# Kernel tuning notes

Measured on AMD Instinct MI355X. Metric: run time of the kernel, lower is better.

## Reference

```python
import jax, jax.numpy as jnp
import numpy as np

N, L, H, K, T = 768, 8, 64, 4, 3

def _mlp2(x, w1, b1, w2, b2):
    # Linear -> ReLU -> Linear -> ReLU (matches nn.Sequential in q/k/v MLPs)
    return jax.nn.relu(jax.nn.relu(x @ w1 + b1) @ w2 + b2)

def setup_inputs() -> dict:
    key = jax.random.key(0)
    ks = jax.random.split(key, 20)
    s = 1.0 / np.sqrt(H)
    def lin(k, din, dout):
        return jax.random.uniform(k, (din, dout), jnp.float32, -s, s)
    def bias(k, dout):
        return jax.random.uniform(k, (dout,), jnp.float32, -s, s)
    inp = {
        "h": jax.random.normal(ks[0], (N, L, H), jnp.float32),
        "coord": jax.random.normal(ks[1], (N, L, K, T), jnp.float32),
        "wq1": lin(ks[2], H, H), "bq1": bias(ks[3], H),
        "wq2": lin(ks[4], H, H), "bq2": bias(ks[5], H),
        "wk1": lin(ks[6], H, H), "bk1": bias(ks[7], H),
        "wk2": lin(ks[8], H, H), "bk2": bias(ks[9], H),
        "wv1": lin(ks[10], H, H), "bv1": bias(ks[11], H),
        "wv2": lin(ks[12], H, H), "bv2": bias(ks[13], H),
        "wc1": lin(ks[14], H, H), "bc1": bias(ks[15], H),
        # final coord layer: Linear(H, 4, bias=False), xavier gain=0.001
        "wc2": jax.random.normal(ks[16], (H, K), jnp.float32) * 0.001,
    }
    return inp

def reference(h, coord, wq1, bq1, wq2, bq2, wk1, bk1, wk2, bk2,
              wv1, bv1, wv2, bv2, wc1, bc1, wc2):
    q = _mlp2(h, wq1, bq1, wq2, bq2)          # [N, L, H]
    k = _mlp2(h, wk1, bk1, wk2, bk2)          # [N, L, H]
    v = _mlp2(h, wv1, bv1, wv2, bv2)          # [N, L, H]
    # scores[i, j, l] = <q_i, k_j> per frame l; softmax over neighbor axis j (dim=1)
    scores = jnp.einsum('ilh,jlh->ijl', q, k)
    alpha = jax.nn.softmax(scores, axis=1)     # [N, N, L]
    h_agg = jnp.einsum('ijl,jlh->ilh', alpha, v)
    cmv = jax.nn.relu(v @ wc1 + bc1) @ wc2     # coord_mlp(v): [N, L, 4]
    coord_diff = coord[:, None] - coord[None]  # [N, N, L, 4, 3]
    x_agg = jnp.einsum('ijlkt,ijl,jlk->ilkt', coord_diff, alpha, cmv)
    return (h + h_agg, coord + x_agg)
```

## Files before the change

kernel.cpp:

```cpp
#include <hip/hip_runtime.h>
#include <hip/hip_bf16.h>

#define NN 768
#define LL 8
#define HH 64
#define IT 16
#define SCP 772
#define ABP 776

typedef __attribute__((ext_vector_type(8))) short bf16x8;
typedef __attribute__((ext_vector_type(4))) float f32x4;

__device__ __forceinline__ short f2bf(float x) {
    union { __hip_bfloat16 h; short s; } u;
    u.h = __float2bfloat16(x);
    return u.s;
}

__device__ __forceinline__ void layer2r(const float (*IN)[68], int k0, int c4,
                                        const float* __restrict__ W,
                                        const float* __restrict__ b,
                                        float4 res[2]) {
    float4 acc[2] = {{0,0,0,0},{0,0,0,0}};
    #pragma unroll
    for (int kk = 0; kk < 16; ++kk) {
        const int k = k0 + kk;
        const float4 wv = *(const float4*)&W[k * 64 + c4];
        #pragma unroll
        for (int rr = 0; rr < 2; ++rr) {
            const float xv = IN[rr][k];
            acc[rr].x = fmaf(xv, wv.x, acc[rr].x);
            acc[rr].y = fmaf(xv, wv.y, acc[rr].y);
            acc[rr].z = fmaf(xv, wv.z, acc[rr].z);
            acc[rr].w = fmaf(xv, wv.w, acc[rr].w);
        }
    }
    const float4 bb = *(const float4*)&b[c4];
    #pragma unroll
    for (int rr = 0; rr < 2; ++rr) {
        acc[rr].x += __shfl_xor(acc[rr].x, 16, 64);
        acc[rr].x += __shfl_xor(acc[rr].x, 32, 64);
        acc[rr].y += __shfl_xor(acc[rr].y, 16, 64);
        acc[rr].y += __shfl_xor(acc[rr].y, 32, 64);
        acc[rr].z += __shfl_xor(acc[rr].z, 16, 64);
        acc[rr].z += __shfl_xor(acc[rr].z, 32, 64);
        acc[rr].w += __shfl_xor(acc[rr].w, 16, 64);
        acc[rr].w += __shfl_xor(acc[rr].w, 32, 64);
        res[rr].x = fmaxf(acc[rr].x + bb.x, 0.f);
        res[rr].y = fmaxf(acc[rr].y + bb.y, 0.f);
        res[rr].z = fmaxf(acc[rr].z + bb.z, 0.f);
        res[rr].w = fmaxf(acc[rr].w + bb.w, 0.f);
    }
}

__global__ __launch_bounds__(256) void qkv_kernel(
    const float* __restrict__ h, const float* __restrict__ coord,
    const float* __restrict__ wq1, const float* __restrict__ bq1,
    const float* __restrict__ wq2, const float* __restrict__ bq2,
    const float* __restrict__ wk1, const float* __restrict__ bk1,
    const float* __restrict__ wk2, const float* __restrict__ bk2,
    const float* __restrict__ wv1, const float* __restrict__ bv1,
    const float* __restrict__ wv2, const float* __restrict__ bv2,
    const float* __restrict__ wc1, const float* __restrict__ bc1,
    const float* __restrict__ wc2,
    short* __restrict__ q_ws, short* __restrict__ k_ws,
    short* __restrict__ vT_ws, short* __restrict__ UT_ws)
{
    const int lane  = threadIdx.x & 63;
    const int w     = threadIdx.x >> 6;
    const int wid   = blockIdx.x * 4 + w;
    const int chain = wid / 3072;
    const int rg    = wid - chain * 3072;
    const int r0    = rg * 2;

    const int c4   = (lane & 15) * 4;
    const int ks   = (lane >> 4) & 3;
    const int k0   = ks * 16;
    const bool lead = (ks == 0);

    __shared__ float As[4][2][68];
    __shared__ float Bs[4][2][68];
    float (*A)[68] = As[w];
    float (*B)[68] = Bs[w];

    {
        const int row = lane >> 5;
        const int c2  = (lane & 31) * 2;
        *(float2*)&A[row][c2] = *(const float2*)&h[(r0 + row) * 64 + c2];
    }
    __builtin_amdgcn_wave_barrier();

    float4 res[2];

    if (chain == 0) {
        layer2r(A, k0, c4, wq1, bq1, res);
        if (lead) {
            *(float4*)&B[0][c4] = res[0];
            *(float4*)&B[1][c4] = res[1];
        }
        __builtin_amdgcn_wave_barrier();
        layer2r(B, k0, c4, wq2, bq2, res);
        if (lead) {
            #pragma unroll
            for (int rr = 0; rr < 2; ++rr) {
                const int g = r0 + rr, i = g >> 3, l = g & 7;
                short4 s;
                s.x = f2bf(res[rr].x); s.y = f2bf(res[rr].y);
                s.z = f2bf(res[rr].z); s.w = f2bf(res[rr].w);
                *(short4*)&q_ws[(l * NN + i) * 64 + c4] = s;
            }
        }
    } else if (chain == 1) {
        layer2r(A, k0, c4, wk1, bk1, res);
        if (lead) {
            *(float4*)&B[0][c4] = res[0];
            *(float4*)&B[1][c4] = res[1];
        }
        __builtin_amdgcn_wave_barrier();
        layer2r(B, k0, c4, wk2, bk2, res);
        if (lead) {
            #pragma unroll
            for (int rr = 0; rr < 2; ++rr) {
                const int g = r0 + rr, i = g >> 3, l = g & 7;
                short4 s;
                s.x = f2bf(res[rr].x); s.y = f2bf(res[rr].y);
                s.z = f2bf(res[rr].z); s.w = f2bf(res[rr].w);
                *(short4*)&k_ws[(l * NN + i) * 64 + c4] = s;
            }
        }
    } else {
        layer2r(A, k0, c4, wv1, bv1, res);
        if (lead) {
            *(float4*)&B[0][c4] = res[0];
            *(float4*)&B[1][c4] = res[1];
        }
        __builtin_amdgcn_wave_barrier();
        layer2r(B, k0, c4, wv2, bv2, res);
        if (lead) {
            #pragma unroll
            for (int rr = 0; rr < 2; ++rr) {
                const int g = r0 + rr, i = g >> 3, l = g & 7;
                vT_ws[((size_t)l * 64 + c4 + 0) * NN + i] = f2bf(res[rr].x);
                vT_ws[((size_t)l * 64 + c4 + 1) * NN + i] = f2bf(res[rr].y);
                vT_ws[((size_t)l * 64 + c4 + 2) * NN + i] = f2bf(res[rr].z);
                vT_ws[((size_t)l * 64 + c4 + 3) * NN + i] = f2bf(res[rr].w);
                *(float4*)&A[rr][c4] = res[rr];
            }
        }
        __builtin_amdgcn_wave_barrier();
        layer2r(A, k0, c4, wc1, bc1, res);
        if (lead) {
            *(float4*)&B[0][c4] = res[0];
            *(float4*)&B[1][c4] = res[1];
        }
        __builtin_amdgcn_wave_barrier();
        {
            const int row = lane >> 5;
            const int rem = lane & 31;
            const int kk  = rem >> 3;
            const int seg = rem & 7;
            float p = 0.f;
            #pragma unroll
            for (int k2 = 0; k2 < 8; ++k2) {
                const int k = seg * 8 + k2;
                p = fmaf(B[row][k], wc2[k * 4 + kk], p);
            }
            p += __shfl_xor(p, 1, 64);
            p += __shfl_xor(p, 2, 64);
            p += __shfl_xor(p, 4, 64);
            if (seg < 4) {
                const int g = r0 + row, i = g >> 3, l = g & 7;
                const float uval =
                    (seg == 0) ? p : p * coord[g * 12 + kk * 3 + (seg - 1)];
                UT_ws[((size_t)l * 16 + kk * 4 + seg) * NN + i] = f2bf(uval);
            }
        }
    }
}

__global__ __launch_bounds__(256) void attn_kernel(
    const short* __restrict__ q_ws, const short* __restrict__ k_ws,
    const short* __restrict__ vT_ws, const short* __restrict__ UT_ws,
    const float* __restrict__ h, const float* __restrict__ coord,
    float* __restrict__ h_out, float* __restrict__ x_out)
{
    const int l    = blockIdx.x & 7;
    const int i0   = (blockIdx.x >> 3) * IT;
    const int t    = threadIdx.x;
    const int lane = t & 63;
    const int w    = t >> 6;
    const int m    = lane & 15;
    const int quad = lane >> 4;

    __shared__ float sc[IT][SCP];
    __shared__ alignas(16) short al[IT][ABP];
    __shared__ float rinv_s[IT];
    __shared__ float part3[4][IT][16];
    __shared__ float smS[IT][16];

    const bf16x8 aq0 = *(const bf16x8*)&q_ws[((size_t)l * NN + i0 + m) * 64 + quad * 8];
    const bf16x8 aq1 = *(const bf16x8*)&q_ws[((size_t)l * NN + i0 + m) * 64 + 32 + quad * 8];

    {
        const short* kl = k_ws + (size_t)l * NN * 64;
        for (int nt = 0; nt < 12; ++nt) {
            const int jb = 192 * w + nt * 16;
            const short* krow = kl + (size_t)(jb + m) * 64;
            bf16x8 b0 = *(const bf16x8*)(krow + quad * 8);
            bf16x8 b1 = *(const bf16x8*)(krow + 32 + quad * 8);
            f32x4 d = {0.f, 0.f, 0.f, 0.f};
            d = __builtin_amdgcn_mfma_f32_16x16x32_bf16(aq0, b0, d, 0, 0, 0);
            d = __builtin_amdgcn_mfma_f32_16x16x32_bf16(aq1, b1, d, 0, 0, 0);
            #pragma unroll
            for (int rg = 0; rg < 4; ++rg)
                sc[quad * 4 + rg][jb + m] = d[rg];
        }
    }
    __syncthreads();

    {
        const int r = t >> 4, sub = t & 15;
        float4 v[12];
        #pragma unroll
        for (int jj = 0; jj < 12; ++jj)
            v[jj] = *(const float4*)&sc[r][sub * 4 + 64 * jj];
        float mx = -1e30f;
        #pragma unroll
        for (int jj = 0; jj < 12; ++jj)
            mx = fmaxf(mx, fmaxf(fmaxf(v[jj].x, v[jj].y),
                                 fmaxf(v[jj].z, v[jj].w)));
        mx = fmaxf(mx, __shfl_xor(mx, 1, 64));
        mx = fmaxf(mx, __shfl_xor(mx, 2, 64));
        mx = fmaxf(mx, __shfl_xor(mx, 4, 64));
        mx = fmaxf(mx, __shfl_xor(mx, 8, 64));
        float s = 0.f;
        #pragma unroll
        for (int jj = 0; jj < 12; ++jj) {
            const float e0 = __expf(v[jj].x - mx);
            const float e1 = __expf(v[jj].y - mx);
            const float e2 = __expf(v[jj].z - mx);
            const float e3 = __expf(v[jj].w - mx);
            s += (e0 + e1) + (e2 + e3);
            short4 p;
            p.x = f2bf(e0); p.y = f2bf(e1); p.z = f2bf(e2); p.w = f2bf(e3);
            *(short4*)&al[r][sub * 4 + 64 * jj] = p;
        }
        s += __shfl_xor(s, 1, 64);
        s += __shfl_xor(s, 2, 64);
        s += __shfl_xor(s, 4, 64);
        s += __shfl_xor(s, 8, 64);
        if (sub == 0) rinv_s[r] = 1.f / s;
    }
    __syncthreads();

    {
        f32x4 acc0 = {0.f, 0.f, 0.f, 0.f};
        f32x4 acc1 = {0.f, 0.f, 0.f, 0.f};
        const short* vrow = vT_ws + ((size_t)l * 64 + 16 * w + m) * NN;
        #pragma unroll 4
        for (int kt = 0; kt < 24; kt += 2) {
            const int ka = kt * 32, kb = ka + 32;
            bf16x8 a0 = *(const bf16x8*)&al[m][ka + quad * 8];
            bf16x8 b0 = *(const bf16x8*)(vrow + ka + quad * 8);
            bf16x8 a1 = *(const bf16x8*)&al[m][kb + quad * 8];
            bf16x8 b1 = *(const bf16x8*)(vrow + kb + quad * 8);
            acc0 = __builtin_amdgcn_mfma_f32_16x16x32_bf16(a0, b0, acc0, 0, 0, 0);
            acc1 = __builtin_amdgcn_mfma_f32_16x16x32_bf16(a1, b1, acc1, 0, 0, 0);
        }
        const int c = 16 * w + m;
        #pragma unroll
        for (int rg = 0; rg < 4; ++rg) {
            const int i = quad * 4 + rg;
            const int row = ((i0 + i) * 8 + l) * 64 + c;
            h_out[row] = h[row] + rinv_s[i] * (acc0[rg] + acc1[rg]);
        }
    }

    {
        f32x4 acc = {0.f, 0.f, 0.f, 0.f};
        const short* urow = UT_ws + ((size_t)l * 16 + m) * NN + 192 * w;
        #pragma unroll
        for (int kt = 0; kt < 6; ++kt) {
            const int k0 = kt * 32;
            bf16x8 a = *(const bf16x8*)&al[m][192 * w + k0 + quad * 8];
            bf16x8 b = *(const bf16x8*)(urow + k0 + quad * 8);
            acc = __builtin_amdgcn_mfma_f32_16x16x32_bf16(a, b, acc, 0, 0, 0);
        }
        #pragma unroll
        for (int rg = 0; rg < 4; ++rg)
            part3[w][quad * 4 + rg][m] = acc[rg];
    }
    __syncthreads();
    {
        const int i = t >> 4, u = t & 15;
        smS[i][u] = (part3[0][i][u] + part3[1][i][u] +
                     part3[2][i][u] + part3[3][i][u]) * rinv_s[i];
    }
    __syncthreads();
    if (t < 192) {
        const int i4 = t / 12, kt = t % 12, k4 = kt / 3, s4 = kt % 3;
        const int idx = ((i0 + i4) * 8 + l) * 12 + kt;
        const float cd = coord[idx];
        x_out[idx] = cd + cd * smS[i4][k4 * 4] - smS[i4][k4 * 4 + 1 + s4];
    }
}

extern "C" void kernel_launch(void* const* d_in, const int* in_sizes, int n_in,
                              void* d_out, int out_size, void* d_ws, size_t ws_size,
                              hipStream_t stream) {
    const float* h     = (const float*)d_in[0];
    const float* coord = (const float*)d_in[1];

    float* h_out = (float*)d_out;
    float* x_out = h_out + NN * LL * HH;

    short* q_ws  = (short*)d_ws;
    short* k_ws  = q_ws + NN * LL * HH;
    short* vT_ws = k_ws + NN * LL * HH;
    short* UT_ws = vT_ws + NN * LL * HH;

    qkv_kernel<<<2304, 256, 0, stream>>>(
        h, coord,
        (const float*)d_in[2],  (const float*)d_in[3],
        (const float*)d_in[4],  (const float*)d_in[5],
        (const float*)d_in[6],  (const float*)d_in[7],
        (const float*)d_in[8],  (const float*)d_in[9],
        (const float*)d_in[10], (const float*)d_in[11],
        (const float*)d_in[12], (const float*)d_in[13],
        (const float*)d_in[14], (const float*)d_in[15],
        (const float*)d_in[16],
        q_ws, k_ws, vT_ws, UT_ws);

    attn_kernel<<<(NN / IT) * LL, 256, 0, stream>>>(
        q_ws, k_ws, vT_ws, UT_ws, h, coord, h_out, x_out);
}
```

Baseline: 122.6 us.

## Compute QKV and coord MLPs with bf16 MFMA using pre-transposed bf16 weights

Replaces the scalar FMA-and-shuffle MLP layers in the QKV kernel with 16x16x32 bf16 MFMA tiles, each wave handling 16 rows instead of 2. A new prep kernel transposes and converts all weight matrices to bf16, and pads the final 64x4 coord layer to 16 columns. The goal is to cut the FP32 ALU work and the cross-lane reductions of the projection stage. In exchange it adds an extra launch, rounds weights and hidden activations to bf16 (lower precision than the prior fp32 path), and makes the global stores more scattered.

```diff
diff --git a/kernel.cpp b/kernel.cpp
--- a/kernel.cpp
+++ b/kernel.cpp
@@ -7,6 +7,7 @@
 #define IT 16
 #define SCP 772
 #define ABP 776
+#define XST 80
 
 typedef __attribute__((ext_vector_type(8))) short bf16x8;
 typedef __attribute__((ext_vector_type(4))) float f32x4;
@@ -17,161 +18,186 @@
     return u.s;
 }
 
-__device__ __forceinline__ void layer2r(const float (*IN)[68], int k0, int c4,
-                                        const float* __restrict__ W,
-                                        const float* __restrict__ b,
-                                        float4 res[2]) {
-    float4 acc[2] = {{0,0,0,0},{0,0,0,0}};
+__device__ __forceinline__ bf16x8 pack8(float4 lo, float4 hi) {
+    bf16x8 r;
+    r[0] = f2bf(lo.x); r[1] = f2bf(lo.y); r[2] = f2bf(lo.z); r[3] = f2bf(lo.w);
+    r[4] = f2bf(hi.x); r[5] = f2bf(hi.y); r[6] = f2bf(hi.z); r[7] = f2bf(hi.w);
+    return r;
+}
+
+__global__ __launch_bounds__(256) void prep_kernel(
+    const float* __restrict__ wq1, const float* __restrict__ wq2,
+    const float* __restrict__ wk1, const float* __restrict__ wk2,
+    const float* __restrict__ wv1, const float* __restrict__ wv2,
+    const float* __restrict__ wc1, const float* __restrict__ wc2,
+    short* __restrict__ WT)
+{
+    const int idx = blockIdx.x * 256 + threadIdx.x;
+    if (idx < 28672) {
+        const int mm = idx >> 12, rem = idx & 4095;
+        const int n = rem >> 6, kk = rem & 63;
+        const float* srcs[7] = {wq1, wq2, wk1, wk2, wv1, wv2, wc1};
+        WT[idx] = f2bf(srcs[mm][kk * 64 + n]);
+    } else if (idx < 29696) {
+        const int rem = idx - 28672;
+        const int n = rem >> 6, kk = rem & 63;
+        WT[idx] = (n < 4) ? f2bf(wc2[kk * 4 + n]) : (short)0;
+    }
+}
+
+__device__ __forceinline__ void layer_mfma(bf16x8 a0, bf16x8 a1,
+                                           const short* __restrict__ WT,
+                                           const float* __restrict__ bias,
+                                           int m, int quad, bool do_relu,
+                                           f32x4 dout[4])
+{
     #pragma unroll
-    for (int kk = 0; kk < 16; ++kk) {
-        const int k = k0 + kk;
-        const float4 wv = *(const float4*)&W[k * 64 + c4];
-        #pragma unroll
-        for (int rr = 0; rr < 2; ++rr) {
-            const float xv = IN[rr][k];
-            acc[rr].x = fmaf(xv, wv.x, acc[rr].x);
-            acc[rr].y = fmaf(xv, wv.y, acc[rr].y);
-            acc[rr].z = fmaf(xv, wv.z, acc[rr].z);
-            acc[rr].w = fmaf(xv, wv.w, acc[rr].w);
-        }
-    }
-    const float4 bb = *(const float4*)&b[c4];
+    for (int nt = 0; nt < 4; ++nt) {
+        const short* wp = WT + (nt * 16 + m) * 64 + quad * 8;
+        bf16x8 b0 = *(const bf16x8*)wp;
+        bf16x8 b1 = *(const bf16x8*)(wp + 32);
+        f32x4 d = {0.f, 0.f, 0.f, 0.f};
+        d = __builtin_amdgcn_mfma_f32_16x16x32_bf16(a0, b0, d, 0, 0, 0);
+        d = __builtin_amdgcn_mfma_f32_16x16x32_bf16(a1, b1, d, 0, 0, 0);
+        if (bias) {
+            const float bb = bias[nt * 16 + m];
+            #pragma unroll
+            for (int rg = 0; rg < 4; ++rg) d[rg] += bb;
+        }
+        if (do_relu) {
+            #pragma unroll
+            for (int rg = 0; rg < 4; ++rg) d[rg] = fmaxf(d[rg], 0.f);
+        }
+        dout[nt] = d;
+    }
+}
+
+__device__ __forceinline__ void d_to_X(const f32x4 d[4], short (*X)[XST],
+                                       int m, int quad) {
     #pragma unroll
-    for (int rr = 0; rr < 2; ++rr) {
-        acc[rr].x += __shfl_xor(acc[rr].x, 16, 64);
-        acc[rr].x += __shfl_xor(acc[rr].x, 32, 64);
-        acc[rr].y += __shfl_xor(acc[rr].y, 16, 64);
-        acc[rr].y += __shfl_xor(acc[rr].y, 32, 64);
-        acc[rr].z += __shfl_xor(acc[rr].z, 16, 64);
-        acc[rr].z += __shfl_xor(acc[rr].z, 32, 64);
-        acc[rr].w += __shfl_xor(acc[rr].w, 16, 64);
-        acc[rr].w += __shfl_xor(acc[rr].w, 32, 64);
-        res[rr].x = fmaxf(acc[rr].x + bb.x, 0.f);
-        res[rr].y = fmaxf(acc[rr].y + bb.y, 0.f);
-        res[rr].z = fmaxf(acc[rr].z + bb.z, 0.f);
-        res[rr].w = fmaxf(acc[rr].w + bb.w, 0.f);
-    }
+    for (int nt = 0; nt < 4; ++nt)
+        #pragma unroll
+        for (int rg = 0; rg < 4; ++rg)
+            X[quad * 4 + rg][nt * 16 + m] = f2bf(d[nt][rg]);
 }
 
 __global__ __launch_bounds__(256) void qkv_kernel(
     const float* __restrict__ h, const float* __restrict__ coord,
-    const float* __restrict__ wq1, const float* __restrict__ bq1,
-    const float* __restrict__ wq2, const float* __restrict__ bq2,
-    const float* __restrict__ wk1, const float* __restrict__ bk1,
-    const float* __restrict__ wk2, const float* __restrict__ bk2,
-    const float* __restrict__ wv1, const float* __restrict__ bv1,
-    const float* __restrict__ wv2, const float* __restrict__ bv2,
-    const float* __restrict__ wc1, const float* __restrict__ bc1,
-    const float* __restrict__ wc2,
+    const float* __restrict__ bq1, const float* __restrict__ bq2,
+    const float* __restrict__ bk1, const float* __restrict__ bk2,
+    const float* __restrict__ bv1, const float* __restrict__ bv2,
+    const float* __restrict__ bc1,
+    const short* __restrict__ WT,
     short* __restrict__ q_ws, short* __restrict__ k_ws,
     short* __restrict__ vT_ws, short* __restrict__ UT_ws)
 {
-    const int lane  = threadIdx.x & 63;
-    const int w     = threadIdx.x >> 6;
-    const int wid   = blockIdx.x * 4 + w;
-    const int chain = wid / 3072;
-    const int rg    = wid - chain * 3072;
-    const int r0    = rg * 2;
-
-    const int c4   = (lane & 15) * 4;
-    const int ks   = (lane >> 4) & 3;
-    const int k0   = ks * 16;
-    const bool lead = (ks == 0);
-
-    __shared__ float As[4][2][68];
-    __shared__ float Bs[4][2][68];
-    float (*A)[68] = As[w];
-    float (*B)[68] = Bs[w];
-
-    {
-        const int row = lane >> 5;
-        const int c2  = (lane & 31) * 2;
-        *(float2*)&A[row][c2] = *(const float2*)&h[(r0 + row) * 64 + c2];
-    }
-    __builtin_amdgcn_wave_barrier();
-
-    float4 res[2];
+    const int lane = threadIdx.x & 63;
+    const int w    = threadIdx.x >> 6;
+    const int wid  = blockIdx.x * 4 + w;
+    const int chain = wid / 384;
+    const int rt    = wid - chain * 384;
+    const int r0    = rt * 16;
+
+    const int m    = lane & 15;
+    const int quad = lane >> 4;
+
+    __shared__ short Xs[4][16][XST];
+    __shared__ float cms[4][16][4];
+    short (*X)[XST] = Xs[w];
+
+    const short* WT_q1 = WT;
+    const short* WT_q2 = WT + 4096;
+    const short* WT_k1 = WT + 8192;
+    const short* WT_k2 = WT + 12288;
+    const short* WT_v1 = WT + 16384;
+    const short* WT_v2 = WT + 20480;
+    const short* WT_c1 = WT + 24576;
+    const short* WT_c2 = WT + 28672;
+
+    bf16x8 a0, a1;
+    {
+        const float* hrow = h + (size_t)(r0 + m) * 64;
+        a0 = pack8(*(const float4*)(hrow + quad * 8),
+                   *(const float4*)(hrow + quad * 8 + 4));
+        a1 = pack8(*(const float4*)(hrow + 32 + quad * 8),
+                   *(const float4*)(hrow + 32 + quad * 8 + 4));
+    }
+
+    f32x4 d[4];
 
     if (chain == 0) {
-        layer2r(A, k0, c4, wq1, bq1, res);
-        if (lead) {
-            *(float4*)&B[0][c4] = res[0];
-            *(float4*)&B[1][c4] = res[1];
-        }
-        __builtin_amdgcn_wave_barrier();
-        layer2r(B, k0, c4, wq2, bq2, res);
-        if (lead) {
-            #pragma unroll
-            for (int rr = 0; rr < 2; ++rr) {
-                const int g = r0 + rr, i = g >> 3, l = g & 7;
-                short4 s;
-                s.x = f2bf(res[rr].x); s.y = f2bf(res[rr].y);
-                s.z = f2bf(res[rr].z); s.w = f2bf(res[rr].w);
-                *(short4*)&q_ws[(l * NN + i) * 64 + c4] = s;
-            }
-        }
+        layer_mfma(a0, a1, WT_q1, bq1, m, quad, true, d);
+        d_to_X(d, X, m, quad);
+        __builtin_amdgcn_wave_barrier();
+        a0 = *(const bf16x8*)&X[m][quad * 8];
+        a1 = *(const bf16x8*)&X[m][32 + quad * 8];
+        layer_mfma(a0, a1, WT_q2, bq2, m, quad, true, d);
+        #pragma unroll
+        for (int nt = 0; nt < 4; ++nt)
+            #pragma unroll
+            for (int rg = 0; rg < 4; ++rg) {
+                const int g = r0 + quad * 4 + rg, i = g >> 3, l = g & 7;
+                q_ws[(l * NN + i) * 64 + nt * 16 + m] = f2bf(d[nt][rg]);
+            }
     } else if (chain == 1) {
-        layer2r(A, k0, c4, wk1, bk1, res);
-        if (lead) {
-            *(float4*)&B[0][c4] = res[0];
-            *(float4*)&B[1][c4] = res[1];
-        }
-        __builtin_amdgcn_wave_barrier();
-        layer2r(B, k0, c4, wk2, bk2, res);
-        if (lead) {
-            #pragma unroll
-            for (int rr = 0; rr < 2; ++rr) {
-                const int g = r0 + rr, i = g >> 3, l = g & 7;
-                short4 s;
-                s.x = f2bf(res[rr].x); s.y = f2bf(res[rr].y);
-                s.z = f2bf(res[rr].z); s.w = f2bf(res[rr].w);
-                *(short4*)&k_ws[(l * NN + i) * 64 + c4] = s;
-            }
-        }
+        layer_mfma(a0, a1, WT_k1, bk1, m, quad, true, d);
+        d_to_X(d, X, m, quad);
+        __builtin_amdgcn_wave_barrier();
+        a0 = *(const bf16x8*)&X[m][quad * 8];
+        a1 = *(const bf16x8*)&X[m][32 + quad * 8];
+        layer_mfma(a0, a1, WT_k2, bk2, m, quad, true, d);
+        #pragma unroll
+        for (int nt = 0; nt < 4; ++nt)
+            #pragma unroll
+            for (int rg = 0; rg < 4; ++rg) {
+                const int g = r0 + quad * 4 + rg, i = g >> 3, l = g & 7;
+                k_ws[(l * NN + i) * 64 + nt * 16 + m] = f2bf(d[nt][rg]);
+            }
     } else {
-        layer2r(A, k0, c4, wv1, bv1, res);
-        if (lead) {
-            *(float4*)&B[0][c4] = res[0];
-            *(float4*)&B[1][c4] = res[1];
-        }
-        __builtin_amdgcn_wave_barrier();
-        layer2r(B, k0, c4, wv2, bv2, res);
-        if (lead) {
-            #pragma unroll
-            for (int rr = 0; rr < 2; ++rr) {
-                const int g = r0 + rr, i = g >> 3, l = g & 7;
-                vT_ws[((size_t)l * 64 + c4 + 0) * NN + i] = f2bf(res[rr].x);
-                vT_ws[((size_t)l * 64 + c4 + 1) * NN + i] = f2bf(res[rr].y);
-                vT_ws[((size_t)l * 64 + c4 + 2) * NN + i] = f2bf(res[rr].z);
-                vT_ws[((size_t)l * 64 + c4 + 3) * NN + i] = f2bf(res[rr].w);
-                *(float4*)&A[rr][c4] = res[rr];
-            }
-        }
-        __builtin_amdgcn_wave_barrier();
-        layer2r(A, k0, c4, wc1, bc1, res);
-        if (lead) {
-            *(float4*)&B[0][c4] = res[0];
-            *(float4*)&B[1][c4] = res[1];
-        }
-        __builtin_amdgcn_wave_barrier();
+        layer_mfma(a0, a1, WT_v1, bv1, m, quad, true, d);
+        d_to_X(d, X, m, quad);
+        __builtin_amdgcn_wave_barrier();
+        a0 = *(const bf16x8*)&X[m][quad * 8];
+        a1 = *(const bf16x8*)&X[m][32 + quad * 8];
+        layer_mfma(a0, a1, WT_v2, bv2, m, quad, true, d);
+        #pragma unroll
+        for (int nt = 0; nt < 4; ++nt)
+            #pragma unroll
+            for (int rg = 0; rg < 4; ++rg) {
+                const int g = r0 + quad * 4 + rg, i = g >> 3, l = g & 7;
+                vT_ws[((size_t)l * 64 + nt * 16 + m) * NN + i] = f2bf(d[nt][rg]);
+            }
+        d_to_X(d, X, m, quad);
+        __builtin_amdgcn_wave_barrier();
+        a0 = *(const bf16x8*)&X[m][quad * 8];
+        a1 = *(const bf16x8*)&X[m][32 + quad * 8];
+        layer_mfma(a0, a1, WT_c1, bc1, m, quad, true, d);
+        d_to_X(d, X, m, quad);
+        __builtin_amdgcn_wave_barrier();
+        a0 = *(const bf16x8*)&X[m][quad * 8];
+        a1 = *(const bf16x8*)&X[m][32 + quad * 8];
         {
-            const int row = lane >> 5;
-            const int rem = lane & 31;
-            const int kk  = rem >> 3;
-            const int seg = rem & 7;
-            float p = 0.f;
-            #pragma unroll
-            for (int k2 = 0; k2 < 8; ++k2) {
-                const int k = seg * 8 + k2;
-                p = fmaf(B[row][k], wc2[k * 4 + kk], p);
-            }
-            p += __shfl_xor(p, 1, 64);
-            p += __shfl_xor(p, 2, 64);
-            p += __shfl_xor(p, 4, 64);
-            if (seg < 4) {
-                const int g = r0 + row, i = g >> 3, l = g & 7;
-                const float uval =
-                    (seg == 0) ? p : p * coord[g * 12 + kk * 3 + (seg - 1)];
+            const short* wp = WT_c2 + m * 64 + quad * 8;
+            bf16x8 b0 = *(const bf16x8*)wp;
+            bf16x8 b1 = *(const bf16x8*)(wp + 32);
+            f32x4 dc = {0.f, 0.f, 0.f, 0.f};
+            dc = __builtin_amdgcn_mfma_f32_16x16x32_bf16(a0, b0, dc, 0, 0, 0);
+            dc = __builtin_amdgcn_mfma_f32_16x16x32_bf16(a1, b1, dc, 0, 0, 0);
+            if (m < 4) {
+                #pragma unroll
+                for (int rg = 0; rg < 4; ++rg)
+                    cms[w][quad * 4 + rg][m] = dc[rg];
+            }
+        }
+        __builtin_amdgcn_wave_barrier();
+        {
+            const int row = lane >> 2, kk = lane & 3;
+            const float c = cms[w][row][kk];
+            const int g = r0 + row, i = g >> 3, l = g & 7;
+            UT_ws[((size_t)l * 16 + kk * 4 + 0) * NN + i] = f2bf(c);
+            #pragma unroll
+            for (int seg = 1; seg < 4; ++seg) {
+                const float uval = c * coord[g * 12 + kk * 3 + (seg - 1)];
                 UT_ws[((size_t)l * 16 + kk * 4 + seg) * NN + i] = f2bf(uval);
             }
         }
@@ -318,18 +344,21 @@
     short* k_ws  = q_ws + NN * LL * HH;
     short* vT_ws = k_ws + NN * LL * HH;
     short* UT_ws = vT_ws + NN * LL * HH;
-
-    qkv_kernel<<<2304, 256, 0, stream>>>(
+    short* WT    = UT_ws + NN * LL * 16;
+
+    prep_kernel<<<116, 256, 0, stream>>>(
+        (const float*)d_in[2],  (const float*)d_in[4],
+        (const float*)d_in[6],  (const float*)d_in[8],
+        (const float*)d_in[10], (const float*)d_in[12],
+        (const float*)d_in[14], (const float*)d_in[16], WT);
+
+    qkv_kernel<<<288, 256, 0, stream>>>(
         h, coord,
-        (const float*)d_in[2],  (const float*)d_in[3],
-        (const float*)d_in[4],  (const float*)d_in[5],
-        (const float*)d_in[6],  (const float*)d_in[7],
-        (const float*)d_in[8],  (const float*)d_in[9],
-        (const float*)d_in[10], (const float*)d_in[11],
-        (const float*)d_in[12], (const float*)d_in[13],
-        (const float*)d_in[14], (const float*)d_in[15],
-        (const float*)d_in[16],
-        q_ws, k_ws, vT_ws, UT_ws);
+        (const float*)d_in[3],  (const float*)d_in[5],
+        (const float*)d_in[7],  (const float*)d_in[9],
+        (const float*)d_in[11], (const float*)d_in[13],
+        (const float*)d_in[15],
+        WT, q_ws, k_ws, vT_ws, UT_ws);
 
     attn_kernel<<<(NN / IT) * LL, 256, 0, stream>>>(
         q_ws, k_ws, vT_ws, UT_ws, h, coord, h_out, x_out);
```

New measurement: 114.8 us. 6.4% less time.
